# Kernel optimization log

Hardware: AMD Instinct MI355X
Metric: run time of the kernel (lower is better)

## Reference

```python
import jax, jax.numpy as jnp
import numpy as np

N_NODES = 100000


def gcn_conv(x, edge_index, W, b, n_nodes):
    # PyG GCNConv: x' = D^{-1/2} (A + I) D^{-1/2} (X W) + b
    xw = x @ W  # [N, out]
    # add self loops
    loops = jnp.arange(n_nodes, dtype=edge_index.dtype)
    row = jnp.concatenate([edge_index[0], loops])  # source
    col = jnp.concatenate([edge_index[1], loops])  # target (aggregation index)
    # symmetric degree normalization based on target degree (with self loops)
    deg = jax.ops.segment_sum(jnp.ones_like(col, dtype=xw.dtype), col,
                              num_segments=n_nodes)
    dinv = jnp.where(deg > 0, jax.lax.rsqrt(deg), 0.0)
    norm = dinv[row] * dinv[col]  # [E+N]
    msgs = norm[:, None] * xw[row]  # [E+N, out]
    out = jax.ops.segment_sum(msgs, col, num_segments=n_nodes)
    return out + b


def setup_inputs() -> dict:
    key = jax.random.key(0)
    k1, k2, k3, k4 = jax.random.split(key, 4)
    N, F_in, H, C, E = N_NODES, 128, 16, 10, 3200000
    x = jax.random.normal(k1, (N, F_in), dtype=jnp.float32)
    edge_index = jax.random.randint(k2, (2, E), 0, N, dtype=jnp.int64)
    W1 = jax.random.normal(k3, (F_in, H), dtype=jnp.float32) / np.sqrt(F_in)
    b1 = jnp.zeros((H,), dtype=jnp.float32)
    W2 = jax.random.normal(k4, (H, C), dtype=jnp.float32) / np.sqrt(H)
    b2 = jnp.zeros((C,), dtype=jnp.float32)
    return {"x": x, "edge_index": edge_index, "W1": W1, "b1": b1,
            "W2": W2, "b2": b2}


def reference(x, edge_index, W1, b1, W2, b2):
    n = x.shape[0]
    h = jax.nn.relu(gcn_conv(x, edge_index, W1, b1, n))
    # dropout is identity in eval mode
    logits = gcn_conv(h, edge_index, W2, b2, n)
    return jax.nn.log_softmax(logits, axis=1)
```

## Files before the change

### kernel.cpp

```cpp
#include <hip/hip_runtime.h>
#include <hip/hip_bf16.h>
#include <math.h>

#define F_IN 128
#define HID  16
#define NCLS 10
#define BS   256
#define CH   16384
#define KPL  4

typedef unsigned int uint;
typedef unsigned short ushort;
typedef __attribute__((ext_vector_type(8))) short short8v;
typedef __attribute__((ext_vector_type(4))) float f32x4;

static __device__ __forceinline__ short f2bf(float f) {
    __hip_bfloat16 h = __float2bfloat16(f);
    return *reinterpret_cast<short*>(&h);
}
static __device__ __forceinline__ float bflo(uint u) {
    union { uint x; float f; } c; c.x = u << 16; return c.f;
}
static __device__ __forceinline__ float bfhi(uint u) {
    union { uint x; float f; } c; c.x = u & 0xffff0000u; return c.f;
}
static __device__ __forceinline__ uint packbf(float f0, float f1) {
    return (uint)(ushort)f2bf(f0) | ((uint)(ushort)f2bf(f1) << 16);
}

__global__ __launch_bounds__(1024) void k_hist2(const int* __restrict__ col, int* __restrict__ hist,
                                                int E, int nbv, int nchunk) {
    extern __shared__ int h[];
    int t = threadIdx.x, k = blockIdx.x;
    for (int i = t; i < nbv; i += 1024) h[i] = 0;
    __syncthreads();
    int start = k * CH, end = min(start + CH, E);
    for (int i = start + t; i < end; i += 1024) atomicAdd(&h[col[i] >> 8], 1);
    __syncthreads();
    for (int i = t; i < nbv; i += 1024) hist[(size_t)i * nchunk + k] = h[i];
}

__global__ void k_cscan(int* __restrict__ hist, int* __restrict__ bcnt, int nchunk, int nbv) {
    int wave = threadIdx.x >> 6, lane = threadIdx.x & 63;
    int b = blockIdx.x * 4 + wave;
    if (b >= nbv) return;
    int* hb = hist + (size_t)b * nchunk;
    int vals[KPL];
    int ls = 0;
    #pragma unroll
    for (int i = 0; i < KPL; ++i) {
        int k = lane * KPL + i;
        vals[i] = (k < nchunk) ? hb[k] : 0;
        ls += vals[i];
    }
    int inc = ls;
    #pragma unroll
    for (int d = 1; d < 64; d <<= 1) {
        int v = __shfl_up(inc, d, 64);
        if (lane >= d) inc += v;
    }
    int run = inc - ls;
    #pragma unroll
    for (int i = 0; i < KPL; ++i) {
        int k = lane * KPL + i;
        if (k < nchunk) { hb[k] = run; run += vals[i]; }
    }
    if (lane == 63) bcnt[b] = inc;
}

__global__ void k_bscan(const int* __restrict__ bcnt, int* __restrict__ boff, int nbv, int E) {
    __shared__ int s[512];
    int t = threadIdx.x;
    int v = (t < nbv) ? bcnt[t] : 0;
    s[t] = v;
    __syncthreads();
    for (int ofs = 1; ofs < 512; ofs <<= 1) {
        int val = (t >= ofs) ? s[t - ofs] : 0;
        __syncthreads();
        if (t >= ofs) s[t] += val;
        __syncthreads();
    }
    if (t < nbv) boff[t] = s[t] - v;
    if (t == nbv) boff[t] = E;
}

__global__ __launch_bounds__(1024) void k_binW(const int* __restrict__ row, const int* __restrict__ col,
                                               const int* __restrict__ hist, const int* __restrict__ boff,
                                               uint* __restrict__ pairs, int E, int nbv, int nchunk) {
    extern __shared__ int lds[];
    int* gbase = lds;
    int* cur   = lds + nbv;
    int t = threadIdx.x, k = blockIdx.x;
    for (int i = t; i < nbv; i += 1024) {
        gbase[i] = boff[i] + hist[(size_t)i * nchunk + k];
        cur[i] = 0;
    }
    __syncthreads();
    int start = k * CH, end = min(start + CH, E);
    for (int i = start + t; i < end; i += 1024) {
        int c = col[i];
        int b = c >> 8;
        int rk = atomicAdd(&cur[b], 1);
        pairs[gbase[b] + rk] = ((uint)row[i] << 8) | (uint)(c & (BS - 1));
    }
}

__global__ __launch_bounds__(1024) void k_nsp(const uint* __restrict__ pairs,
                                              const int* __restrict__ boff,
                                              int* __restrict__ off, float* __restrict__ dinv,
                                              int* __restrict__ srow, int N, int nbv, int E) {
    __shared__ int c[BS];
    __shared__ int s[BS];
    int b = blockIdx.x, t = threadIdx.x;
    if (t < BS) c[t] = 0;
    __syncthreads();
    int st = boff[b], en = boff[b + 1];
    for (int i = st + t; i < en; i += 1024) atomicAdd(&c[pairs[i] & (BS - 1)], 1);
    __syncthreads();
    int v = 0;
    if (t < BS) { v = c[t]; s[t] = v; }
    __syncthreads();
    for (int ofs = 1; ofs < BS; ofs <<= 1) {
        int val = 0;
        if (t < BS && t >= ofs) val = s[t - ofs];
        __syncthreads();
        if (t < BS && t >= ofs) s[t] += val;
        __syncthreads();
    }
    int mybase = 0;
    if (t < BS) {
        mybase = st + s[t] - v;
        int n = (b << 8) + t;
        if (n < N) {
            off[n] = mybase;
            dinv[n] = rsqrtf((float)v + 1.0f);
        }
    }
    if (b == nbv - 1 && t == 0) off[N] = E;
    __syncthreads();
    if (t < BS) { c[t] = mybase; s[t] = 0; }
    __syncthreads();
    for (int i = st + t; i < en; i += 1024) {
        uint pv = pairs[i];
        int cl = pv & (BS - 1);
        int p = c[cl] + atomicAdd(&s[cl], 1);
        srow[p] = (int)(pv >> 8);
    }
}

__global__ void k_xwm(const float* __restrict__ x, const float* __restrict__ W1,
                      const float* __restrict__ dinv, __hip_bfloat16* __restrict__ xws, int N) {
    int w = threadIdx.x >> 6, l = threadIdx.x & 63;
    int n0 = (blockIdx.x * 4 + w) * 16;
    if (n0 >= N) return;
    int h = l & 15;
    int kb8 = (l >> 4) << 3;
    short8v bfrag[4];
    #pragma unroll
    for (int kk = 0; kk < 4; ++kk) {
        #pragma unroll
        for (int j = 0; j < 8; ++j) {
            int k = kk * 32 + kb8 + j;
            bfrag[kk][j] = f2bf(W1[k * HID + h]);
        }
    }
    int rrow = n0 + h;
    const float* xr = x + (size_t)rrow * F_IN + kb8;
    f32x4 acc = {0.f, 0.f, 0.f, 0.f};
    #pragma unroll
    for (int kk = 0; kk < 4; ++kk) {
        const float4* p = reinterpret_cast<const float4*>(xr + kk * 32);
        float4 lo = p[0], hi = p[1];
        short8v a;
        a[0] = f2bf(lo.x); a[1] = f2bf(lo.y); a[2] = f2bf(lo.z); a[3] = f2bf(lo.w);
        a[4] = f2bf(hi.x); a[5] = f2bf(hi.y); a[6] = f2bf(hi.z); a[7] = f2bf(hi.w);
        acc = __builtin_amdgcn_mfma_f32_16x16x32_bf16(a, bfrag[kk], acc, 0, 0, 0);
    }
    #pragma unroll
    for (int j = 0; j < 4; ++j) {
        int n = n0 + ((l >> 4) << 2) + j;
        xws[(size_t)n * HID + h] = __float2bfloat16(acc[j] * dinv[n]);
    }
}

__global__ void k_agg1(const uint* __restrict__ xws32, const int* __restrict__ off,
                       const int* __restrict__ srow, const float* __restrict__ dinv,
                       const float* __restrict__ b1, uint* __restrict__ hs32, int N) {
    int gid = blockIdx.x * blockDim.x + threadIdx.x;
    int n = gid >> 3;
    int p = threadIdx.x & 7;
    if (n >= N) return;
    int s = off[n], e = off[n + 1];
    uint v = xws32[(size_t)n * 8 + p];
    float a0 = bflo(v), b0 = bfhi(v);
    float a1 = 0.f, b1a = 0.f, a2 = 0.f, b2a = 0.f, a3 = 0.f, b3a = 0.f;
    int i = s;
    for (; i + 7 < e; i += 8) {
        int r0 = srow[i],     r1 = srow[i + 1], r2 = srow[i + 2], r3 = srow[i + 3];
        int r4 = srow[i + 4], r5 = srow[i + 5], r6 = srow[i + 6], r7 = srow[i + 7];
        uint v0 = xws32[(size_t)r0 * 8 + p], v1 = xws32[(size_t)r1 * 8 + p];
        uint v2 = xws32[(size_t)r2 * 8 + p], v3 = xws32[(size_t)r3 * 8 + p];
        uint v4 = xws32[(size_t)r4 * 8 + p], v5 = xws32[(size_t)r5 * 8 + p];
        uint v6 = xws32[(size_t)r6 * 8 + p], v7 = xws32[(size_t)r7 * 8 + p];
        a0 += bflo(v0); b0 += bfhi(v0);  a1 += bflo(v1); b1a += bfhi(v1);
        a2 += bflo(v2); b2a += bfhi(v2); a3 += bflo(v3); b3a += bfhi(v3);
        a0 += bflo(v4); b0 += bfhi(v4);  a1 += bflo(v5); b1a += bfhi(v5);
        a2 += bflo(v6); b2a += bfhi(v6); a3 += bflo(v7); b3a += bfhi(v7);
    }
    for (; i < e; ++i) {
        uint vv = xws32[(size_t)srow[i] * 8 + p];
        a0 += bflo(vv); b0 += bfhi(vv);
    }
    float sl = (a0 + a1) + (a2 + a3);
    float sh = (b0 + b1a) + (b2a + b3a);
    float d = dinv[n];
    float h0 = d * sl + b1[2 * p];
    float h1 = d * sh + b1[2 * p + 1];
    h0 = h0 > 0.f ? h0 : 0.f;
    h1 = h1 > 0.f ? h1 : 0.f;
    hs32[(size_t)n * 8 + p] = packbf(d * h0, d * h1);
}

__global__ void k_agg2(const uint* __restrict__ hs32, const int* __restrict__ off,
                       const int* __restrict__ srow, const float* __restrict__ dinv,
                       const float* __restrict__ W2, const float* __restrict__ b2,
                       float* __restrict__ out, int N) {
    __shared__ float gs[32][17];
    __shared__ float W2s[HID * NCLS];
    __shared__ float b2s[NCLS];
    int t = threadIdx.x;
    if (t < HID * NCLS) W2s[t] = W2[t];
    if (t < NCLS) b2s[t] = b2[t];
    int grp = t >> 3, p = t & 7;
    int n = blockIdx.x * 32 + grp;
    float g0 = 0.f, g1 = 0.f;
    if (n < N) {
        int s = off[n], e = off[n + 1];
        uint v = hs32[(size_t)n * 8 + p];
        float a0 = bflo(v), b0 = bfhi(v);
        float a1 = 0.f, b1a = 0.f, a2 = 0.f, b2a = 0.f, a3 = 0.f, b3a = 0.f;
        int i = s;
        for (; i + 7 < e; i += 8) {
            int r0 = srow[i],     r1 = srow[i + 1], r2 = srow[i + 2], r3 = srow[i + 3];
            int r4 = srow[i + 4], r5 = srow[i + 5], r6 = srow[i + 6], r7 = srow[i + 7];
            uint v0 = hs32[(size_t)r0 * 8 + p], v1 = hs32[(size_t)r1 * 8 + p];
            uint v2 = hs32[(size_t)r2 * 8 + p], v3 = hs32[(size_t)r3 * 8 + p];
            uint v4 = hs32[(size_t)r4 * 8 + p], v5 = hs32[(size_t)r5 * 8 + p];
            uint v6 = hs32[(size_t)r6 * 8 + p], v7 = hs32[(size_t)r7 * 8 + p];
            a0 += bflo(v0); b0 += bfhi(v0);  a1 += bflo(v1); b1a += bfhi(v1);
            a2 += bflo(v2); b2a += bfhi(v2); a3 += bflo(v3); b3a += bfhi(v3);
            a0 += bflo(v4); b0 += bfhi(v4);  a1 += bflo(v5); b1a += bfhi(v5);
            a2 += bflo(v6); b2a += bfhi(v6); a3 += bflo(v7); b3a += bfhi(v7);
        }
        for (; i < e; ++i) {
            uint vv = hs32[(size_t)srow[i] * 8 + p];
            a0 += bflo(vv); b0 += bfhi(vv);
        }
        float d = dinv[n];
        g0 = d * ((a0 + a1) + (a2 + a3));
        g1 = d * ((b0 + b1a) + (b2a + b3a));
    }
    gs[grp][2 * p]     = g0;
    gs[grp][2 * p + 1] = g1;
    __syncthreads();
    if (t < 32) {
        int n2 = blockIdx.x * 32 + t;
        if (n2 < N) {
            float v[NCLS];
            float m = -INFINITY;
            #pragma unroll
            for (int c = 0; c < NCLS; ++c) {
                float a = b2s[c];
                #pragma unroll
                for (int j = 0; j < HID; ++j) a += gs[t][j] * W2s[j * NCLS + c];
                v[c] = a;
                m = fmaxf(m, a);
            }
            float ssum = 0.f;
            #pragma unroll
            for (int c = 0; c < NCLS; ++c) ssum += __expf(v[c] - m);
            float lse = m + __logf(ssum);
            #pragma unroll
            for (int c = 0; c < NCLS; ++c) out[(size_t)n2 * NCLS + c] = v[c] - lse;
        }
    }
}

extern "C" void kernel_launch(void* const* d_in, const int* in_sizes, int n_in,
                              void* d_out, int out_size, void* d_ws, size_t ws_size,
                              hipStream_t stream) {
    const float* x  = (const float*)d_in[0];
    const int*   ei = (const int*)d_in[1];
    const float* W1 = (const float*)d_in[2];
    const float* b1 = (const float*)d_in[3];
    const float* W2 = (const float*)d_in[4];
    const float* b2 = (const float*)d_in[5];
    float* out = (float*)d_out;

    const int N = in_sizes[0] / F_IN;
    const int E = in_sizes[1] / 2;
    const int* row = ei;
    const int* col = ei + E;

    const int nbv = (N + BS - 1) / BS;
    const int nchunk = (E + CH - 1) / CH;

    char* ws = (char*)d_ws;
    auto alignup = [](size_t v) { return (v + 255) & ~(size_t)255; };
    size_t offb = 0;
    int*   hist = (int*)  (ws + offb); offb += alignup((size_t)nbv * nchunk * 4);
    int*   bcnt = (int*)  (ws + offb); offb += alignup((size_t)(nbv + 1) * 4);
    int*   boff = (int*)  (ws + offb); offb += alignup((size_t)(nbv + 1) * 4);
    int*   off  = (int*)  (ws + offb); offb += alignup((size_t)(N + 1) * 4);
    float* dinv = (float*)(ws + offb); offb += alignup((size_t)N * 4);
    uint*  pairs= (uint*) (ws + offb); offb += alignup((size_t)E * 4);
    int*   srow = (int*)  (ws + offb); offb += alignup((size_t)E * 4);
    uint*  xws  = (uint*) (ws + offb); offb += alignup((size_t)N * HID * 2);
    uint*  hs   = (uint*) (ws + offb); offb += alignup((size_t)N * HID * 2);
    (void)ws_size; (void)n_in; (void)out_size;

    size_t histB = (size_t)nbv * 4;
    const int nxb = ((N / 16) + 3) / 4;

    k_hist2<<<nchunk, 1024, histB,     stream>>>(col, hist, E, nbv, nchunk);
    k_cscan<<<(nbv + 3) / 4, 256, 0,   stream>>>(hist, bcnt, nchunk, nbv);
    k_bscan<<<1, 512, 0,               stream>>>(bcnt, boff, nbv, E);
    k_binW <<<nchunk, 1024, 2 * histB, stream>>>(row, col, hist, boff, pairs, E, nbv, nchunk);
    k_nsp  <<<nbv, 1024, 0,            stream>>>(pairs, boff, off, dinv, srow, N, nbv, E);
    k_xwm  <<<nxb, 256, 0,             stream>>>(x, W1, dinv, (__hip_bfloat16*)xws, N);
    k_agg1 <<<(N * 8 + 255) / 256, 256, 0, stream>>>(xws, off, srow, dinv, b1, hs, N);
    k_agg2 <<<(N * 8 + 255) / 256, 256, 0, stream>>>(hs, off, srow, dinv, W2, b2, out, N);
}
```

Measured before the change: 123.8 us.

## Fuse bucket scan into binning kernels, vectorize loads, cache pairs in LDS

After: 126.9 us. +2.5%, slower.

```diff
diff --git a/kernel.cpp b/kernel.cpp
--- a/kernel.cpp
+++ b/kernel.cpp
@@ -6,8 +6,9 @@
 #define HID  16
 #define NCLS 10
 #define BS   256
-#define CH   16384
-#define KPL  4
+#define CH   12288
+#define KPL  5
+#define LDSCAP 10240
 
 typedef unsigned int uint;
 typedef unsigned short ushort;
@@ -35,7 +36,16 @@
     for (int i = t; i < nbv; i += 1024) h[i] = 0;
     __syncthreads();
     int start = k * CH, end = min(start + CH, E);
-    for (int i = start + t; i < end; i += 1024) atomicAdd(&h[col[i] >> 8], 1);
+    int cnt4 = (end - start) >> 2;
+    const int4* col4 = (const int4*)(col + start);
+    for (int i = t; i < cnt4; i += 1024) {
+        int4 c4 = col4[i];
+        atomicAdd(&h[c4.x >> 8], 1);
+        atomicAdd(&h[c4.y >> 8], 1);
+        atomicAdd(&h[c4.z >> 8], 1);
+        atomicAdd(&h[c4.w >> 8], 1);
+    }
+    for (int i = start + (cnt4 << 2) + t; i < end; i += 1024) atomicAdd(&h[col[i] >> 8], 1);
     __syncthreads();
     for (int i = t; i < nbv; i += 1024) hist[(size_t)i * nchunk + k] = h[i];
 }
@@ -68,36 +78,46 @@
     if (lane == 63) bcnt[b] = inc;
 }
 
-__global__ void k_bscan(const int* __restrict__ bcnt, int* __restrict__ boff, int nbv, int E) {
-    __shared__ int s[512];
-    int t = threadIdx.x;
-    int v = (t < nbv) ? bcnt[t] : 0;
-    s[t] = v;
-    __syncthreads();
-    for (int ofs = 1; ofs < 512; ofs <<= 1) {
-        int val = (t >= ofs) ? s[t - ofs] : 0;
-        __syncthreads();
-        if (t >= ofs) s[t] += val;
-        __syncthreads();
-    }
-    if (t < nbv) boff[t] = s[t] - v;
-    if (t == nbv) boff[t] = E;
-}
-
 __global__ __launch_bounds__(1024) void k_binW(const int* __restrict__ row, const int* __restrict__ col,
-                                               const int* __restrict__ hist, const int* __restrict__ boff,
+                                               const int* __restrict__ hist, const int* __restrict__ bcnt,
                                                uint* __restrict__ pairs, int E, int nbv, int nchunk) {
     extern __shared__ int lds[];
     int* gbase = lds;
     int* cur   = lds + nbv;
+    int* sc    = lds + 2 * nbv;
     int t = threadIdx.x, k = blockIdx.x;
-    for (int i = t; i < nbv; i += 1024) {
-        gbase[i] = boff[i] + hist[(size_t)i * nchunk + k];
-        cur[i] = 0;
+    if (t < 512) sc[t] = (t < nbv) ? bcnt[t] : 0;
+    __syncthreads();
+    for (int ofs = 1; ofs < 512; ofs <<= 1) {
+        int val = 0;
+        if (t < 512 && t >= ofs) val = sc[t - ofs];
+        __syncthreads();
+        if (t < 512 && t >= ofs) sc[t] += val;
+        __syncthreads();
+    }
+    if (t < nbv) {
+        gbase[t] = (t ? sc[t - 1] : 0) + hist[(size_t)t * nchunk + k];
+        cur[t] = 0;
     }
     __syncthreads();
     int start = k * CH, end = min(start + CH, E);
-    for (int i = start + t; i < end; i += 1024) {
+    int cnt4 = (end - start) >> 2;
+    const int4* col4 = (const int4*)(col + start);
+    const int4* row4 = (const int4*)(row + start);
+    for (int i = t; i < cnt4; i += 1024) {
+        int4 c4 = col4[i];
+        int4 r4 = row4[i];
+        int b0 = c4.x >> 8, b1 = c4.y >> 8, b2 = c4.z >> 8, b3 = c4.w >> 8;
+        int k0 = atomicAdd(&cur[b0], 1);
+        int k1 = atomicAdd(&cur[b1], 1);
+        int k2 = atomicAdd(&cur[b2], 1);
+        int k3 = atomicAdd(&cur[b3], 1);
+        pairs[gbase[b0] + k0] = ((uint)r4.x << 8) | (uint)(c4.x & (BS - 1));
+        pairs[gbase[b1] + k1] = ((uint)r4.y << 8) | (uint)(c4.y & (BS - 1));
+        pairs[gbase[b2] + k2] = ((uint)r4.z << 8) | (uint)(c4.z & (BS - 1));
+        pairs[gbase[b3] + k3] = ((uint)r4.w << 8) | (uint)(c4.w & (BS - 1));
+    }
+    for (int i = start + (cnt4 << 2) + t; i < end; i += 1024) {
         int c = col[i];
         int b = c >> 8;
         int rk = atomicAdd(&cur[b], 1);
@@ -106,16 +126,31 @@
 }
 
 __global__ __launch_bounds__(1024) void k_nsp(const uint* __restrict__ pairs,
-                                              const int* __restrict__ boff,
+                                              const int* __restrict__ bcnt,
                                               int* __restrict__ off, float* __restrict__ dinv,
                                               int* __restrict__ srow, int N, int nbv, int E) {
     __shared__ int c[BS];
     __shared__ int s[BS];
+    __shared__ int sc[512];
+    __shared__ uint pc[LDSCAP];
     int b = blockIdx.x, t = threadIdx.x;
+    if (t < 512) sc[t] = (t < nbv) ? bcnt[t] : 0;
     if (t < BS) c[t] = 0;
     __syncthreads();
-    int st = boff[b], en = boff[b + 1];
-    for (int i = st + t; i < en; i += 1024) atomicAdd(&c[pairs[i] & (BS - 1)], 1);
+    for (int ofs = 1; ofs < 512; ofs <<= 1) {
+        int val = 0;
+        if (t < 512 && t >= ofs) val = sc[t - ofs];
+        __syncthreads();
+        if (t < 512 && t >= ofs) sc[t] += val;
+        __syncthreads();
+    }
+    int st = b ? sc[b - 1] : 0;
+    int en = sc[b];
+    for (int i = st + t; i < en; i += 1024) {
+        uint pv = pairs[i];
+        if (i - st < LDSCAP) pc[i - st] = pv;
+        atomicAdd(&c[pv & (BS - 1)], 1);
+    }
     __syncthreads();
     int v = 0;
     if (t < BS) { v = c[t]; s[t] = v; }
@@ -141,7 +176,7 @@
     if (t < BS) { c[t] = mybase; s[t] = 0; }
     __syncthreads();
     for (int i = st + t; i < en; i += 1024) {
-        uint pv = pairs[i];
+        uint pv = (i - st < LDSCAP) ? pc[i - st] : pairs[i];
         int cl = pv & (BS - 1);
         int p = c[cl] + atomicAdd(&s[cl], 1);
         srow[p] = (int)(pv >> 8);
@@ -310,7 +345,6 @@
     size_t offb = 0;
     int*   hist = (int*)  (ws + offb); offb += alignup((size_t)nbv * nchunk * 4);
     int*   bcnt = (int*)  (ws + offb); offb += alignup((size_t)(nbv + 1) * 4);
-    int*   boff = (int*)  (ws + offb); offb += alignup((size_t)(nbv + 1) * 4);
     int*   off  = (int*)  (ws + offb); offb += alignup((size_t)(N + 1) * 4);
     float* dinv = (float*)(ws + offb); offb += alignup((size_t)N * 4);
     uint*  pairs= (uint*) (ws + offb); offb += alignup((size_t)E * 4);
@@ -320,13 +354,13 @@
     (void)ws_size; (void)n_in; (void)out_size;
 
     size_t histB = (size_t)nbv * 4;
+    size_t binB  = (size_t)(2 * nbv + 512) * 4;
     const int nxb = ((N / 16) + 3) / 4;
 
     k_hist2<<<nchunk, 1024, histB,     stream>>>(col, hist, E, nbv, nchunk);
     k_cscan<<<(nbv + 3) / 4, 256, 0,   stream>>>(hist, bcnt, nchunk, nbv);
-    k_bscan<<<1, 512, 0,               stream>>>(bcnt, boff, nbv, E);
-    k_binW <<<nchunk, 1024, 2 * histB, stream>>>(row, col, hist, boff, pairs, E, nbv, nchunk);
-    k_nsp  <<<nbv, 1024, 0,            stream>>>(pairs, boff, off, dinv, srow, N, nbv, E);
+    k_binW <<<nchunk, 1024, binB,      stream>>>(row, col, hist, bcnt, pairs, E, nbv, nchunk);
+    k_nsp  <<<nbv, 1024, 0,            stream>>>(pairs, bcnt, off, dinv, srow, N, nbv, E);
     k_xwm  <<<nxb, 256, 0,             stream>>>(x, W1, dinv, (__hip_bfloat16*)xws, N);
     k_agg1 <<<(N * 8 + 255) / 256, 256, 0, stream>>>(xws, off, srow, dinv, b1, hs, N);
     k_agg2 <<<(N * 8 + 255) / 256, 256, 0, stream>>>(hs, off, srow, dinv, W2, b2, out, N);
```
